# Performance work log

Hardware: AMD Instinct MI355X
Metric: run time of the kernel (lower is better)

## Reference

```python
import jax, jax.numpy as jnp
import numpy as np

B, T, D, H, K, V = 2, 2048, 2048, 16, 128, 128


def _l2norm(x, eps=1e-12):
    # F.normalize(p=2, dim=-1)
    n = jnp.sqrt(jnp.sum(x * x, axis=-1, keepdims=True))
    return x / jnp.maximum(n, eps)


def setup_inputs() -> dict:
    key = jax.random.key(0)
    ks = jax.random.split(key, 7)
    s = D ** -0.5
    return {
        "x": jax.random.normal(ks[0], (B, T, D), jnp.float32),
        "Wq": jax.random.normal(ks[1], (H * K, D), jnp.float32) * s,
        "Wk": jax.random.normal(ks[2], (H * K, D), jnp.float32) * s,
        "Wv": jax.random.normal(ks[3], (H * V, D), jnp.float32) * s,
        "Wa": jax.random.normal(ks[4], (H, D), jnp.float32) * s,
        "ba": jnp.zeros((H,), jnp.float32),
        "Wb": jax.random.normal(ks[5], (H, D), jnp.float32) * s,
        "bb": jnp.zeros((H,), jnp.float32),
    }


def _forward(x, Wq, Wk, Wv, Wa, ba, Wb, bb):
    Bq, Tq, _ = x.shape
    # projections (nn.Linear: y = x @ W.T)
    q = _l2norm(jnp.einsum('btd,od->bto', x, Wq).reshape(Bq, Tq, H, K))
    k = _l2norm(jnp.einsum('btd,od->bto', x, Wk).reshape(Bq, Tq, H, K))
    v = jnp.einsum('btd,od->bto', x, Wv).reshape(Bq, Tq, H, V)
    alpha = jax.nn.sigmoid(jnp.einsum('btd,hd->bth', x, Wa) + ba)          # [B,T,H] decay in (0,1)
    beta = jax.nn.softplus(jnp.einsum('btd,hd->bth', x, Wb) + bb) * K ** (-0.5)

    # gated delta rule recurrence over time (vectorized over B,H):
    #   S_t = a_t * S_{t-1} (I - b_t k_t k_t^T) + b_t v_t k_t^T ;  o_t = S_t q_t
    def step(S, inp):
        q_t, k_t, v_t, a_t, b_t = inp  # [B,H,K],[B,H,K],[B,H,V],[B,H],[B,H]
        Sd = S * a_t[..., None, None]                              # decay  [B,H,V,K]
        pred = jnp.einsum('bhvk,bhk->bhv', Sd, k_t)                # S k
        u = b_t[..., None] * (v_t - pred)                          # delta update [B,H,V]
        S_new = Sd + u[..., None] * k_t[:, :, None, :]             # rank-1 write
        o_t = jnp.einsum('bhvk,bhk->bhv', S_new, q_t)
        return S_new, o_t

    S0 = jnp.zeros((Bq, H, V, K), x.dtype)
    xs = (q.transpose(1, 0, 2, 3), k.transpose(1, 0, 2, 3),
          v.transpose(1, 0, 2, 3), alpha.transpose(1, 0, 2), beta.transpose(1, 0, 2))
    _, o = jax.lax.scan(step, S0, xs)
    return o.transpose(1, 0, 2, 3)  # [B,T,H,V]


def reference(x, Wq, Wk, Wv, Wa, ba, Wb, bb):
    return _forward(x, Wq, Wk, Wv, Wa, ba, Wb, bb)
```

## Files before the change

kernel.cpp:

```cpp
#include <hip/hip_runtime.h>
#include <math.h>

#define BB 2
#define TT 2048
#define DD 2048
#define HH 16
#define KK 128

typedef _Float16 h4 __attribute__((ext_vector_type(4)));
typedef _Float16 v8h __attribute__((ext_vector_type(8)));
typedef float v4f __attribute__((ext_vector_type(4)));

__global__ __launch_bounds__(256) void gemm_nt3(const float* __restrict__ A,
                                                const float* __restrict__ W0,
                                                const float* __restrict__ W1,
                                                const float* __restrict__ W2,
                                                float* __restrict__ Cbase,
                                                int M, int N, int Kd) {
  __shared__ float As[8][128];
  __shared__ float Bs[8][128];
  const int z = blockIdx.z;
  const float* W = (z == 0) ? W0 : (z == 1) ? W1 : W2;
  float* C = Cbase + (size_t)z * M * N;
  const int tid = threadIdx.x;
  const int bm = blockIdx.y * 128;
  const int bn = blockIdx.x * 128;
  const int lrow = tid >> 1;
  const int lcol = (tid & 1) * 4;
  const int rm = (tid >> 4) * 8;
  const int rn = (tid & 15) * 8;
  const float* Ap = A + (size_t)(bm + lrow) * Kd + lcol;
  const float* Wp = W + (size_t)(bn + lrow) * Kd + lcol;
  float acc[8][8];
#pragma unroll
  for (int i = 0; i < 8; i++)
#pragma unroll
    for (int j = 0; j < 8; j++) acc[i][j] = 0.f;
  float4 av = *(const float4*)Ap;
  float4 wv = *(const float4*)Wp;
  for (int d0 = 0; d0 < Kd; d0 += 8) {
    __syncthreads();
    As[lcol + 0][lrow] = av.x; As[lcol + 1][lrow] = av.y;
    As[lcol + 2][lrow] = av.z; As[lcol + 3][lrow] = av.w;
    Bs[lcol + 0][lrow] = wv.x; Bs[lcol + 1][lrow] = wv.y;
    Bs[lcol + 2][lrow] = wv.z; Bs[lcol + 3][lrow] = wv.w;
    __syncthreads();
    if (d0 + 8 < Kd) {
      av = *(const float4*)(Ap + d0 + 8);
      wv = *(const float4*)(Wp + d0 + 8);
    }
#pragma unroll
    for (int kk = 0; kk < 8; kk++) {
      const float4 a0 = *(const float4*)&As[kk][rm];
      const float4 a1 = *(const float4*)&As[kk][rm + 4];
      const float4 b0 = *(const float4*)&Bs[kk][rn];
      const float4 b1 = *(const float4*)&Bs[kk][rn + 4];
      const float ar[8] = {a0.x, a0.y, a0.z, a0.w, a1.x, a1.y, a1.z, a1.w};
      const float br[8] = {b0.x, b0.y, b0.z, b0.w, b1.x, b1.y, b1.z, b1.w};
#pragma unroll
      for (int i = 0; i < 8; i++)
#pragma unroll
        for (int j = 0; j < 8; j++) acc[i][j] = fmaf(ar[i], br[j], acc[i][j]);
    }
  }
#pragma unroll
  for (int i = 0; i < 8; i++) {
    float* cp = C + (size_t)(bm + rm + i) * N + bn + rn;
    float4 c0 = {acc[i][0], acc[i][1], acc[i][2], acc[i][3]};
    float4 c1 = {acc[i][4], acc[i][5], acc[i][6], acc[i][7]};
    *(float4*)cp = c0;
    *(float4*)(cp + 4) = c1;
  }
}

__global__ __launch_bounds__(256) void convert_f16(
    const float* __restrict__ x, const float* __restrict__ Wq,
    const float* __restrict__ Wk, const float* __restrict__ Wv,
    _Float16* __restrict__ xh, _Float16* __restrict__ xl,
    _Float16* __restrict__ Wf) {
  const size_t N4X = (size_t)BB * TT * DD / 4;
  const size_t N4W = (size_t)(HH * KK) * DD / 4;
  const size_t i = (size_t)blockIdx.x * 256 + threadIdx.x;
  if (i < N4X) {
    const float4 v = ((const float4*)x)[i];
    h4 hi, lo;
    hi.x = (_Float16)v.x; hi.y = (_Float16)v.y;
    hi.z = (_Float16)v.z; hi.w = (_Float16)v.w;
    lo.x = (_Float16)(v.x - (float)hi.x);
    lo.y = (_Float16)(v.y - (float)hi.y);
    lo.z = (_Float16)(v.z - (float)hi.z);
    lo.w = (_Float16)(v.w - (float)hi.w);
    ((h4*)xh)[i] = hi;
    ((h4*)xl)[i] = lo;
  } else {
    const size_t j = i - N4X;
    const float* Ws = (j < N4W) ? Wq : (j < 2 * N4W) ? Wk : Wv;
    const size_t jj = (j < N4W) ? j : (j < 2 * N4W) ? (j - N4W) : (j - 2 * N4W);
    const float4 v = ((const float4*)Ws)[jj];
    h4 hi;
    hi.x = (_Float16)v.x; hi.y = (_Float16)v.y;
    hi.z = (_Float16)v.z; hi.w = (_Float16)v.w;
    ((h4*)Wf)[j] = hi;
  }
}

#define GLDS(gp, lp)                                              \
  __builtin_amdgcn_global_load_lds(                               \
      (const __attribute__((address_space(1))) void*)(gp),        \
      (__attribute__((address_space(3))) void*)(lp), 16, 0, 0)

__global__ __launch_bounds__(256) void gemm_mfma(
    const _Float16* __restrict__ xh, const _Float16* __restrict__ xl,
    const _Float16* __restrict__ Wf, float* __restrict__ Cbase) {
  __shared__ float4 lraw[1536];
  _Float16* Ah = (_Float16*)lraw;
  _Float16* Al = Ah + 4096;
  _Float16* Bs = Al + 4096;

  const int z = blockIdx.z;
  const _Float16* W = Wf + (size_t)z * DD * (HH * KK);
  float* C = Cbase + (size_t)z * (BB * TT) * (HH * KK);

  const int tid = threadIdx.x;
  const int w = tid >> 6;
  const int lane = tid & 63;
  const int bm = blockIdx.y * 128;
  const int bn = blockIdx.x * 128;
  const int wm = (w & 1) * 64;
  const int wn = (w >> 1) * 64;
  const int m16 = lane & 15;
  const int quad = lane >> 4;

  const _Float16* gAh = xh + (size_t)(bm + (tid >> 2)) * DD + (tid & 3) * 8;
  const _Float16* gAl = xl + (size_t)(bm + (tid >> 2)) * DD + (tid & 3) * 8;
  const _Float16* gB = W + (size_t)(bn + (tid >> 2)) * DD + (tid & 3) * 8;
  const int lb = w * 512;

  v4f acc[4][4];
#pragma unroll
  for (int i = 0; i < 4; i++)
#pragma unroll
    for (int j = 0; j < 4; j++) acc[i][j] = (v4f){0.f, 0.f, 0.f, 0.f};

  for (int d0 = 0; d0 < DD; d0 += 32) {
    GLDS(gAh + d0, Ah + lb);
    GLDS(gAh + d0 + 64 * DD, Ah + 2048 + lb);
    GLDS(gAl + d0, Al + lb);
    GLDS(gAl + d0 + 64 * DD, Al + 2048 + lb);
    GLDS(gB + d0, Bs + lb);
    GLDS(gB + d0 + 64 * DD, Bs + 2048 + lb);
    __syncthreads();
    v8h ah[4], al[4], bw[4];
#pragma unroll
    for (int i = 0; i < 4; i++) {
      ah[i] = *(const v8h*)&Ah[(wm + i * 16 + m16) * 32 + quad * 8];
      al[i] = *(const v8h*)&Al[(wm + i * 16 + m16) * 32 + quad * 8];
      bw[i] = *(const v8h*)&Bs[(wn + i * 16 + m16) * 32 + quad * 8];
    }
#pragma unroll
    for (int mi = 0; mi < 4; mi++)
#pragma unroll
      for (int ni = 0; ni < 4; ni++) {
        acc[mi][ni] = __builtin_amdgcn_mfma_f32_16x16x32_f16(ah[mi], bw[ni],
                                                             acc[mi][ni], 0, 0, 0);
        acc[mi][ni] = __builtin_amdgcn_mfma_f32_16x16x32_f16(al[mi], bw[ni],
                                                             acc[mi][ni], 0, 0, 0);
      }
    __syncthreads();
  }
#pragma unroll
  for (int mi = 0; mi < 4; mi++) {
#pragma unroll
    for (int r = 0; r < 4; r++) {
      float* cp =
          C + (size_t)(bm + wm + mi * 16 + quad * 4 + r) * (HH * KK) + bn + wn + m16;
#pragma unroll
      for (int ni = 0; ni < 4; ni++) cp[ni * 16] = acc[mi][ni][r];
    }
  }
}

__global__ __launch_bounds__(64) void ab_proj(const float* __restrict__ x,
                                              const float* __restrict__ Wa,
                                              const float* __restrict__ ba,
                                              const float* __restrict__ Wb,
                                              const float* __restrict__ bb,
                                              float* __restrict__ abq) {
  const int row = blockIdx.x;
  const int g = blockIdx.y;
  const int h0 = (g & 1) * 8;
  const bool isA = (g < 2);
  const float* W = isA ? Wa : Wb;
  const int lane = threadIdx.x;
  const float* xr = x + (size_t)row * DD;
  float acc[8];
#pragma unroll
  for (int j = 0; j < 8; j++) acc[j] = 0.f;
  for (int d = lane; d < DD; d += 64) {
    const float xv = xr[d];
#pragma unroll
    for (int j = 0; j < 8; j++)
      acc[j] = fmaf(xv, W[(size_t)(h0 + j) * DD + d], acc[j]);
  }
#pragma unroll
  for (int j = 0; j < 8; j++) {
#pragma unroll
    for (int off = 32; off > 0; off >>= 1) acc[j] += __shfl_xor(acc[j], off, 64);
  }
  if (lane == 0) {
    if (isA) {
#pragma unroll
      for (int j = 0; j < 8; j++) {
        const float z = acc[j] + ba[h0 + j];
        abq[((size_t)row * HH + h0 + j) * 4 + 0] = 1.0f / (1.0f + expf(-z));
      }
    } else {
#pragma unroll
      for (int j = 0; j < 8; j++) {
        const float z = acc[j] + bb[h0 + j];
        const float sp = (z > 20.f) ? z : log1pf(expf(z));
        abq[((size_t)row * HH + h0 + j) * 4 + 1] = sp * 0.08838834764831845f;
      }
    }
  }
}

__global__ __launch_bounds__(256) void norm_qk(float* __restrict__ q,
                                               float* __restrict__ k,
                                               float* __restrict__ abq) {
  const int vec = blockIdx.x * 4 + (threadIdx.x >> 6);
  const int l = threadIdx.x & 63;
  float* qp = q + (size_t)vec * 128;
  float* kp = k + (size_t)vec * 128;
  float q0 = qp[l], q1 = qp[l + 64];
  float k0 = kp[l], k1 = kp[l + 64];
  float sq = q0 * q0 + q1 * q1;
  float sk = k0 * k0 + k1 * k1;
#pragma unroll
  for (int off = 32; off > 0; off >>= 1) {
    sq += __shfl_xor(sq, off, 64);
    sk += __shfl_xor(sk, off, 64);
  }
  const float iq = 1.0f / fmaxf(sqrtf(sq), 1e-12f);
  const float ik = 1.0f / fmaxf(sqrtf(sk), 1e-12f);
  q0 *= iq; q1 *= iq; k0 *= ik; k1 *= ik;
  qp[l] = q0; qp[l + 64] = q1;
  kp[l] = k0; kp[l + 64] = k1;
  float pq = q0 * k0 + q1 * k1;
#pragma unroll
  for (int off = 32; off > 0; off >>= 1) pq += __shfl_xor(pq, off, 64);
  if (l == 0) abq[(size_t)vec * 4 + 2] = pq;
}

#define DPP_ADD(x, ctrl)                                                     \
  ((x) + __int_as_float(__builtin_amdgcn_update_dpp(                         \
             0, __float_as_int(x), (ctrl), 0xF, 0xF, true)))

#define SCAN_STEP(kc0, kc1, qc0, qc1, vc, ac, store_ptr)                       \
  {                                                                            \
    float dkA = fmaf(S0, kc0.x, fmaf(S1, kc0.y, fmaf(S2, kc0.z, S3 * kc0.w))); \
    float dkB = fmaf(S4, kc1.x, fmaf(S5, kc1.y, fmaf(S6, kc1.z, S7 * kc1.w))); \
    float dqA = fmaf(S0, qc0.x, fmaf(S1, qc0.y, fmaf(S2, qc0.z, S3 * qc0.w))); \
    float dqB = fmaf(S4, qc1.x, fmaf(S5, qc1.y, fmaf(S6, qc1.z, S7 * qc1.w))); \
    float dk = dkA + dkB;                                                      \
    float dq = dqA + dqB;                                                      \
    dk = DPP_ADD(dk, 0xB1);  dq = DPP_ADD(dq, 0xB1);             \
    dk = DPP_ADD(dk, 0x4E);  dq = DPP_ADD(dq, 0x4E);             \
    dk = DPP_ADD(dk, 0x141); dq = DPP_ADD(dq, 0x141);            \
    dk = DPP_ADD(dk, 0x140); dq = DPP_ADD(dq, 0x140);            \
    const float u = ac.y * (vc - ac.x * dk);                                   \
    const float oo = fmaf(ac.x, dq, u * ac.z);                                 \
    S0 = fmaf(ac.x, S0, u * kc0.x);                                            \
    S1 = fmaf(ac.x, S1, u * kc0.y);                                            \
    S2 = fmaf(ac.x, S2, u * kc0.z);                                            \
    S3 = fmaf(ac.x, S3, u * kc0.w);                                            \
    S4 = fmaf(ac.x, S4, u * kc1.x);                                            \
    S5 = fmaf(ac.x, S5, u * kc1.y);                                            \
    S6 = fmaf(ac.x, S6, u * kc1.z);                                            \
    S7 = fmaf(ac.x, S7, u * kc1.w);                                            \
    if (g == 0) *(store_ptr) = oo;                                             \
  }

#define PD 8

__global__ __launch_bounds__(256) void scan_kernel(const float* __restrict__ q,
                                                   const float* __restrict__ k,
                                                   const float* __restrict__ v,
                                                   const float* __restrict__ abq,
                                                   float* __restrict__ o) {
  const int bid = blockIdx.x;
  const int bh = bid & 31;
  const int s = bid >> 5;
  const int h = bh & 15;
  const int b = bh >> 4;
  const int tid = threadIdx.x;
  const int w = tid >> 6;
  const int lane = tid & 63;
  const int rg = lane >> 4;
  const int g = lane & 15;
  const int vrow = s * 16 + w * 4 + rg;

  const size_t base = (size_t)b * TT * 2048 + (size_t)h * KK;
  const float* kb = k + base + g * 8;
  const float* qb = q + base + g * 8;
  const float* vb = v + base + vrow;
  const float* ab = abq + ((size_t)b * TT * HH + h) * 4;
  float* ob = o + base + vrow;

  float S0 = 0.f, S1 = 0.f, S2 = 0.f, S3 = 0.f;
  float S4 = 0.f, S5 = 0.f, S6 = 0.f, S7 = 0.f;

  float4 kf0[PD], kf1[PD], qf0[PD], qf1[PD], af[PD];
  float vf[PD];
#pragma unroll
  for (int d = 0; d < PD; d++) {
    kf0[d] = *(const float4*)(kb + d * 2048);
    kf1[d] = *(const float4*)(kb + d * 2048 + 4);
    qf0[d] = *(const float4*)(qb + d * 2048);
    qf1[d] = *(const float4*)(qb + d * 2048 + 4);
    vf[d] = vb[d * 2048];
    af[d] = *(const float4*)(ab + d * 64);
  }

  int off = 0;
  int aoff = 0;
  for (int t0 = 0; t0 < TT - PD; t0 += PD) {
#pragma unroll
    for (int j = 0; j < PD; j++) {
      SCAN_STEP(kf0[j], kf1[j], qf0[j], qf1[j], vf[j], af[j],
                ob + off + j * 2048);
      kf0[j] = *(const float4*)(kb + off + (j + PD) * 2048);
      kf1[j] = *(const float4*)(kb + off + (j + PD) * 2048 + 4);
      qf0[j] = *(const float4*)(qb + off + (j + PD) * 2048);
      qf1[j] = *(const float4*)(qb + off + (j + PD) * 2048 + 4);
      vf[j] = vb[off + (j + PD) * 2048];
      af[j] = *(const float4*)(ab + aoff + (j + PD) * 64);
      __builtin_amdgcn_sched_barrier(0);
    }
    off += PD * 2048;
    aoff += PD * 64;
  }
#pragma unroll
  for (int j = 0; j < PD; j++) {
    SCAN_STEP(kf0[j], kf1[j], qf0[j], qf1[j], vf[j], af[j], ob + off + j * 2048);
  }
}

extern "C" void kernel_launch(void* const* d_in, const int* in_sizes, int n_in,
                              void* d_out, int out_size, void* d_ws,
                              size_t ws_size, hipStream_t stream) {
  const float* x = (const float*)d_in[0];
  const float* Wq = (const float*)d_in[1];
  const float* Wk = (const float*)d_in[2];
  const float* Wv = (const float*)d_in[3];
  const float* Wa = (const float*)d_in[4];
  const float* ba = (const float*)d_in[5];
  const float* Wb = (const float*)d_in[6];
  const float* bb = (const float*)d_in[7];
  float* out = (float*)d_out;
  float* ws = (float*)d_ws;

  const size_t PROJ = (size_t)BB * TT * HH * KK;
  const size_t NABQ = (size_t)BB * TT * HH * 4;
  float* qw = ws;
  float* kw = ws + PROJ;
  float* vw = ws + 2 * PROJ;
  float* abq = ws + 3 * PROJ;
  _Float16* xh = (_Float16*)(abq + NABQ);
  _Float16* xl = xh + (size_t)BB * TT * DD;
  _Float16* Wf = xl + (size_t)BB * TT * DD;
  const size_t NEED = (3 * PROJ + NABQ) * 4 +
                      ((size_t)BB * TT * DD * 2 + 3 * (size_t)(HH * KK) * DD) * 2;

  const int M = BB * TT;
  const int N = HH * KK;
  if (ws_size >= NEED) {
    const int cgrid = (int)(((size_t)BB * TT * DD / 4 + 3 * (size_t)N * DD / 4) / 256);
    convert_f16<<<cgrid, 256, 0, stream>>>(x, Wq, Wk, Wv, xh, xl, Wf);
    gemm_mfma<<<dim3(N / 128, M / 128, 3), 256, 0, stream>>>(xh, xl, Wf, qw);
  } else {
    gemm_nt3<<<dim3(N / 128, M / 128, 3), 256, 0, stream>>>(x, Wq, Wk, Wv, qw,
                                                            M, N, DD);
  }
  ab_proj<<<dim3(M, 4), 64, 0, stream>>>(x, Wa, ba, Wb, bb, abq);
  norm_qk<<<(BB * TT * HH) / 4, 256, 0, stream>>>(qw, kw, abq);
  scan_kernel<<<BB * HH * 8, 256, 0, stream>>>(qw, kw, vw, abq, out);
}
```

Before: 801.2 us.

## Split scan state across 32 lanes per row and double scan grid

Each V-row of the recurrent state is now held by 32 lanes with 4 state elements each, instead of 16 lanes with 8. Each wave therefore covers 2 rows instead of 4, and the grid doubles to 512 blocks. The aim is more parallelism and more waves across CUs, with a shorter per-lane FMA chain on the serial time loop. In exchange, every step needs an extra cross-half shuffle reduction, and each block issues more redundant k/q loads.

```diff
diff --git a/kernel.cpp b/kernel.cpp
--- a/kernel.cpp
+++ b/kernel.cpp
@@ -256,38 +256,31 @@
   ((x) + __int_as_float(__builtin_amdgcn_update_dpp(                         \
              0, __float_as_int(x), (ctrl), 0xF, 0xF, true)))
 
-#define SCAN_STEP(kc0, kc1, qc0, qc1, vc, ac, store_ptr)                       \
+#define SCAN_STEP(kc, qc, vc, ac, store_ptr)                                   \
   {                                                                            \
-    float dkA = fmaf(S0, kc0.x, fmaf(S1, kc0.y, fmaf(S2, kc0.z, S3 * kc0.w))); \
-    float dkB = fmaf(S4, kc1.x, fmaf(S5, kc1.y, fmaf(S6, kc1.z, S7 * kc1.w))); \
-    float dqA = fmaf(S0, qc0.x, fmaf(S1, qc0.y, fmaf(S2, qc0.z, S3 * qc0.w))); \
-    float dqB = fmaf(S4, qc1.x, fmaf(S5, qc1.y, fmaf(S6, qc1.z, S7 * qc1.w))); \
-    float dk = dkA + dkB;                                                      \
-    float dq = dqA + dqB;                                                      \
+    float dk = fmaf(S0, kc.x, fmaf(S1, kc.y, fmaf(S2, kc.z, S3 * kc.w)));      \
+    float dq = fmaf(S0, qc.x, fmaf(S1, qc.y, fmaf(S2, qc.z, S3 * qc.w)));      \
     dk = DPP_ADD(dk, 0xB1);  dq = DPP_ADD(dq, 0xB1);             \
     dk = DPP_ADD(dk, 0x4E);  dq = DPP_ADD(dq, 0x4E);             \
     dk = DPP_ADD(dk, 0x141); dq = DPP_ADD(dq, 0x141);            \
     dk = DPP_ADD(dk, 0x140); dq = DPP_ADD(dq, 0x140);            \
-    const float u = ac.y * (vc - ac.x * dk);                                   \
+    dk += __shfl_xor(dk, 32, 64);                                \
+    dq += __shfl_xor(dq, 32, 64);                                              \
+    const float u = ac.y * fmaf(-ac.x, dk, vc);                                \
     const float oo = fmaf(ac.x, dq, u * ac.z);                                 \
-    S0 = fmaf(ac.x, S0, u * kc0.x);                                            \
-    S1 = fmaf(ac.x, S1, u * kc0.y);                                            \
-    S2 = fmaf(ac.x, S2, u * kc0.z);                                            \
-    S3 = fmaf(ac.x, S3, u * kc0.w);                                            \
-    S4 = fmaf(ac.x, S4, u * kc1.x);                                            \
-    S5 = fmaf(ac.x, S5, u * kc1.y);                                            \
-    S6 = fmaf(ac.x, S6, u * kc1.z);                                            \
-    S7 = fmaf(ac.x, S7, u * kc1.w);                                            \
-    if (g == 0) *(store_ptr) = oo;                                             \
+    S0 = fmaf(ac.x, S0, u * kc.x);                                             \
+    S1 = fmaf(ac.x, S1, u * kc.y);                                             \
+    S2 = fmaf(ac.x, S2, u * kc.z);                                             \
+    S3 = fmaf(ac.x, S3, u * kc.w);                                             \
+    if (ks == 0) *(store_ptr) = oo;                                            \
   }
 
 #define PD 8
 
-__global__ __launch_bounds__(256) void scan_kernel(const float* __restrict__ q,
-                                                   const float* __restrict__ k,
-                                                   const float* __restrict__ v,
-                                                   const float* __restrict__ abq,
-                                                   float* __restrict__ o) {
+__global__ __launch_bounds__(256, 2) void scan_kernel(
+    const float* __restrict__ q, const float* __restrict__ k,
+    const float* __restrict__ v, const float* __restrict__ abq,
+    float* __restrict__ o) {
   const int bid = blockIdx.x;
   const int bh = bid & 31;
   const int s = bid >> 5;
@@ -296,28 +289,25 @@
   const int tid = threadIdx.x;
   const int w = tid >> 6;
   const int lane = tid & 63;
-  const int rg = lane >> 4;
-  const int g = lane & 15;
-  const int vrow = s * 16 + w * 4 + rg;
+  const int rg = (lane >> 4) & 1;
+  const int ks = (lane & 15) | ((lane >> 5) << 4);
+  const int vrow = s * 8 + w * 2 + rg;
 
   const size_t base = (size_t)b * TT * 2048 + (size_t)h * KK;
-  const float* kb = k + base + g * 8;
-  const float* qb = q + base + g * 8;
+  const float* kb = k + base + ks * 4;
+  const float* qb = q + base + ks * 4;
   const float* vb = v + base + vrow;
   const float* ab = abq + ((size_t)b * TT * HH + h) * 4;
   float* ob = o + base + vrow;
 
   float S0 = 0.f, S1 = 0.f, S2 = 0.f, S3 = 0.f;
-  float S4 = 0.f, S5 = 0.f, S6 = 0.f, S7 = 0.f;
-
-  float4 kf0[PD], kf1[PD], qf0[PD], qf1[PD], af[PD];
+
+  float4 kf[PD], qf[PD], af[PD];
   float vf[PD];
 #pragma unroll
   for (int d = 0; d < PD; d++) {
-    kf0[d] = *(const float4*)(kb + d * 2048);
-    kf1[d] = *(const float4*)(kb + d * 2048 + 4);
-    qf0[d] = *(const float4*)(qb + d * 2048);
-    qf1[d] = *(const float4*)(qb + d * 2048 + 4);
+    kf[d] = *(const float4*)(kb + d * 2048);
+    qf[d] = *(const float4*)(qb + d * 2048);
     vf[d] = vb[d * 2048];
     af[d] = *(const float4*)(ab + d * 64);
   }
@@ -327,12 +317,9 @@
   for (int t0 = 0; t0 < TT - PD; t0 += PD) {
 #pragma unroll
     for (int j = 0; j < PD; j++) {
-      SCAN_STEP(kf0[j], kf1[j], qf0[j], qf1[j], vf[j], af[j],
-                ob + off + j * 2048);
-      kf0[j] = *(const float4*)(kb + off + (j + PD) * 2048);
-      kf1[j] = *(const float4*)(kb + off + (j + PD) * 2048 + 4);
-      qf0[j] = *(const float4*)(qb + off + (j + PD) * 2048);
-      qf1[j] = *(const float4*)(qb + off + (j + PD) * 2048 + 4);
+      SCAN_STEP(kf[j], qf[j], vf[j], af[j], ob + off + j * 2048);
+      kf[j] = *(const float4*)(kb + off + (j + PD) * 2048);
+      qf[j] = *(const float4*)(qb + off + (j + PD) * 2048);
       vf[j] = vb[off + (j + PD) * 2048];
       af[j] = *(const float4*)(ab + aoff + (j + PD) * 64);
       __builtin_amdgcn_sched_barrier(0);
@@ -342,7 +329,7 @@
   }
 #pragma unroll
   for (int j = 0; j < PD; j++) {
-    SCAN_STEP(kf0[j], kf1[j], qf0[j], qf1[j], vf[j], af[j], ob + off + j * 2048);
+    SCAN_STEP(kf[j], qf[j], vf[j], af[j], ob + off + j * 2048);
   }
 }
 
@@ -384,5 +371,5 @@
   }
   ab_proj<<<dim3(M, 4), 64, 0, stream>>>(x, Wa, ba, Wb, bb, abq);
   norm_qk<<<(BB * TT * HH) / 4, 256, 0, stream>>>(qw, kw, abq);
-  scan_kernel<<<BB * HH * 8, 256, 0, stream>>>(qw, kw, vw, abq, out);
-}
+  scan_kernel<<<BB * HH * 16, 256, 0, stream>>>(qw, kw, vw, abq, out);
+}
```

New measurement: 1.063 ms. +32.7%, slower.
